# Performance work log

Hardware: AMD Instinct MI355X
Metric: run time of the kernel (lower is better)

The kernel has to match this reference:

```python
import jax, jax.numpy as jnp
import numpy as np
from jax.ops import segment_sum
import math

N = 100_000
E = 1_600_000
D = 128          # node_feature_dim
HID = 128        # hidden_dim
H = 4            # num_heads
HD = HID // H    # head_dim


def setup_inputs() -> dict:
    key = jax.random.key(0)
    ks = jax.random.split(key, 12)
    s = 0.02
    return {
        "node_features": jax.random.normal(ks[0], (N, D), dtype=jnp.float32),
        "edge_index": jax.random.randint(ks[1], (2, E), 0, N, dtype=jnp.int32),
        "edge_weights": jax.random.uniform(ks[2], (E,), dtype=jnp.float32),
        "Wq": jax.random.normal(ks[3], (D, HID), dtype=jnp.float32) * s,
        "bq": jnp.zeros((HID,), dtype=jnp.float32),
        "Wk": jax.random.normal(ks[4], (D, HID), dtype=jnp.float32) * s,
        "bk": jnp.zeros((HID,), dtype=jnp.float32),
        "Wv": jax.random.normal(ks[5], (D, HID), dtype=jnp.float32) * s,
        "bv": jnp.zeros((HID,), dtype=jnp.float32),
        "Wo": jax.random.normal(ks[6], (HID, HID), dtype=jnp.float32) * s,
        "bo": jnp.zeros((HID,), dtype=jnp.float32),
        "We": jax.random.normal(ks[7], (H,), dtype=jnp.float32) * s,  # edge_proj weight, Linear(1, H)
        "be": jnp.zeros((H,), dtype=jnp.float32),
    }


def reference(node_features, edge_index, edge_weights,
              Wq, bq, Wk, bk, Wv, bv, Wo, bo, We, be):
    scale = math.sqrt(HD)
    Q = (node_features @ Wq + bq).reshape(N, H, HD)
    K = (node_features @ Wk + bk).reshape(N, H, HD)
    V = (node_features @ Wv + bv).reshape(N, H, HD)

    src, tgt = edge_index[0], edge_index[1]

    # per-edge attention scores (E, H)
    scores = jnp.einsum("ehd,ehd->eh", Q[tgt], K[src]) / scale
    # edge_proj: Linear(1, H) applied to edge_weights[:, None]
    scores = scores + edge_weights[:, None] * We[None, :] + be[None, :]

    # scatter softmax over target nodes
    max_scores = jnp.full((N, H), -1e9, dtype=scores.dtype).at[tgt].max(scores)
    exp_scores = jnp.exp(scores - max_scores[tgt])
    sum_exp = segment_sum(exp_scores, tgt, num_segments=N)
    probs = exp_scores / (sum_exp[tgt] + 1e-8)

    # weighted scatter-sum aggregation
    out = jnp.zeros((N, H, HD), dtype=scores.dtype).at[tgt].add(probs[:, :, None] * V[src])
    return out.reshape(N, HID) @ Wo + bo
```

## Files before the change

kernel.cpp:

```cpp
#include <hip/hip_runtime.h>

#define N_NODES 100000
#define E_EDGES 1600000

typedef unsigned short u16;
typedef unsigned int   u32;
typedef unsigned char  u8;
typedef float f32x4  __attribute__((ext_vector_type(4)));
typedef short bf16x8 __attribute__((ext_vector_type(8)));

#define NBUK 98
#define BCAP 20480
#define MBLOCKS 1563
#define ECHUNKS 391

__device__ __forceinline__ u16 f2b(float f) {
  u32 b = __float_as_uint(f);
  return (u16)((b + 0x7FFFu + ((b >> 16) & 1u)) >> 16);
}
__device__ __forceinline__ float blo(u32 u) { return __uint_as_float(u << 16); }
__device__ __forceinline__ float bhi(u32 u) { return __uint_as_float(u & 0xFFFF0000u); }

__device__ __forceinline__ u8 f2e4m3(float f) {
  u32 b = __float_as_uint(f);
  u32 s = (b >> 24) & 0x80u;
  float y = __uint_as_float(b & 0x7fffffffu) * 0x1p-120f;
  u32 u = __float_as_uint(y);
  u += 0x7FFFFu + ((u >> 20) & 1u);
  return (u8)(s | ((u >> 20) & 0x7fu));
}

__device__ __forceinline__ float e4m3_1(u32 x) {
  u32 y = ((x & 0x80u) << 24) | ((x & 0x7fu) << 20);
  return __uint_as_float(y) * 0x1p120f;
}

__device__ __forceinline__ void dec4(u32 kq, float& k0, float& k1, float& k2, float& k3) {
#if __has_builtin(__builtin_amdgcn_cvt_pk_f32_fp8)
  auto lo = __builtin_amdgcn_cvt_pk_f32_fp8((int)kq, false);
  auto hi = __builtin_amdgcn_cvt_pk_f32_fp8((int)kq, true);
  k0 = lo[0]; k1 = lo[1]; k2 = hi[0]; k3 = hi[1];
#else
  k0 = e4m3_1(kq); k1 = e4m3_1(kq >> 8); k2 = e4m3_1(kq >> 16); k3 = e4m3_1(kq >> 24);
#endif
}

template<int CTRL>
__device__ __forceinline__ float dpp_add(float d) {
  int x = __builtin_amdgcn_update_dpp(0, __float_as_int(d), CTRL, 0xf, 0xf, true);
  return d + __int_as_float(x);
}
__device__ __forceinline__ float reduce8(float d) {
  d = dpp_add<0xB1>(d);
  d = dpp_add<0x4E>(d);
  d = dpp_add<0x141>(d);
  return d;
}

__global__ __launch_bounds__(256) void setup(
    const float* __restrict__ Wq, const float* __restrict__ Wk,
    const float* __restrict__ Wv, const float* __restrict__ Wo,
    u16* __restrict__ Wt, u32* __restrict__ bcur)
{
  int tid = blockIdx.x * 256 + threadIdx.x;
  if (tid < NBUK) bcur[tid] = (u32)tid * BCAP;
  int idx = tid - NBUK;
  if (idx >= 0 && idx < 65536) {
    int mat = idx >> 14;
    int rem = idx & 16383;
    int n = rem >> 7, k = rem & 127;
    const float* W = (mat == 0) ? Wq : (mat == 1) ? Wk : (mat == 2) ? Wv : Wo;
    Wt[idx] = f2b(W[k * 128 + n]);
  }
}

__global__ __launch_bounds__(256) void qkv_pass1(
    const float* __restrict__ A, const u16* __restrict__ Wt,
    const float* __restrict__ bq, const float* __restrict__ bk,
    const float* __restrict__ bv,
    u16* __restrict__ Qb, u8* __restrict__ Kf8, u16* __restrict__ Vb16, int M,
    const int* __restrict__ ei, const float* __restrict__ ew,
    u32* __restrict__ bcur, uint2* __restrict__ stag)
{
  __shared__ __align__(16) char smem[52224];
  const int t = threadIdx.x;

  if ((int)blockIdx.x < MBLOCKS) {
    typedef u16 row136[136];
    row136* Alds = (row136*)smem;
    row136* Blds = (row136*)(smem + 17408);
    const int row0 = blockIdx.x * 64;

#pragma unroll
    for (int i = 0; i < 8; ++i) {
      int f = t + i * 256;
      int r = f >> 5, c4 = f & 31;
      int gr = row0 + r; if (gr >= M) gr = M - 1;
      float4 v = ((const float4*)(A + (size_t)gr * 128))[c4];
      u32* dst = (u32*)&Alds[r][c4 * 4];
      dst[0] = (u32)f2b(v.x) | ((u32)f2b(v.y) << 16);
      dst[1] = (u32)f2b(v.z) | ((u32)f2b(v.w) << 16);
    }

    const int lane = t & 63;
    const int mrow = lane & 15;
    const int q    = lane >> 4;
    const int m0   = (t >> 6) * 16;

    for (int m = 0; m < 3; ++m) {
      __syncthreads();
#pragma unroll
      for (int i = 0; i < 8; ++i) {
        int f = t + i * 256;
        int r = f >> 4, c8 = f & 15;
        uint4 v = ((const uint4*)(Wt + (size_t)m * 16384 + (size_t)r * 128))[c8];
        *(uint4*)&Blds[r][c8 * 8] = v;
      }
      __syncthreads();

      f32x4 acc[8];
#pragma unroll
      for (int c = 0; c < 8; ++c) acc[c] = (f32x4){0.f, 0.f, 0.f, 0.f};
#pragma unroll
      for (int kk = 0; kk < 4; ++kk) {
        const int kb = kk * 32 + q * 8;
        bf16x8 a = *(const bf16x8*)&Alds[m0 + mrow][kb];
#pragma unroll
        for (int c = 0; c < 8; ++c) {
          bf16x8 b = *(const bf16x8*)&Blds[c * 16 + mrow][kb];
          acc[c] = __builtin_amdgcn_mfma_f32_16x16x32_bf16(a, b, acc[c], 0, 0, 0);
        }
      }

      const float* bias = (m == 0) ? bq : (m == 1) ? bk : bv;
      __syncthreads();
      if (m == 1) {
        u8* Kst = (u8*)Blds;
#pragma unroll
        for (int c = 0; c < 8; ++c) {
          int gcol = c * 16 + mrow;
          float bvv = bias[gcol];
#pragma unroll
          for (int r = 0; r < 4; ++r)
            Kst[(m0 + q * 4 + r) * 128 + gcol] = f2e4m3(acc[c][r] + bvv);
        }
        __syncthreads();
#pragma unroll
        for (int i = 0; i < 2; ++i) {
          int f = t + i * 256;
          int r = f >> 3, c16 = f & 7;
          int grow = row0 + r;
          if (grow < M)
            *(uint4*)(Kf8 + (size_t)grow * 128 + c16 * 16) =
                *(const uint4*)(Kst + r * 128 + c16 * 16);
        }
      } else {
        u16* St = (u16*)Blds;
#pragma unroll
        for (int c = 0; c < 8; ++c) {
          int gcol = c * 16 + mrow;
          float bvv = bias[gcol];
#pragma unroll
          for (int r = 0; r < 4; ++r)
            St[(m0 + q * 4 + r) * 128 + gcol] = f2b(acc[c][r] + bvv);
        }
        __syncthreads();
        u16* dstM = (m == 0) ? Qb : Vb16;
#pragma unroll
        for (int i = 0; i < 4; ++i) {
          int f = t + i * 256;
          int r = f >> 4, c8 = f & 15;
          int grow = row0 + r;
          if (grow < M)
            *(uint4*)(dstM + (size_t)grow * 128 + c8 * 8) =
                *(const uint4*)(St + r * 128 + c8 * 8);
        }
      }
    }
  } else {
    u32* s_px    = (u32*)smem;
    u32* s_py    = (u32*)(smem + 16384);
    u32* s_gp    = (u32*)(smem + 32768);
    u32* s_hist  = (u32*)(smem + 49152);
    u32* s_excl  = (u32*)(smem + 49544);
    u32* s_gbase = (u32*)(smem + 49936);
    u32* s_wsum  = (u32*)(smem + 50328);

    const int base = ((int)blockIdx.x - MBLOCKS) * 4096;
    const int nv = min(4096, E_EDGES - base);

    if (t < NBUK) s_hist[t] = 0;
    __syncthreads();

    u32 tg[16], py[16];
    const int4*   src4 = (const int4*)(ei + base);
    const int4*   tgt4 = (const int4*)(ei + E_EDGES + base);
    const float4* ewv4 = (const float4*)(ew + base);
#pragma unroll
    for (int j = 0; j < 4; ++j) {
      int q4 = t + j * 256;
      bool valid = (q4 * 4) < nv;
      int qq = valid ? q4 : 0;
      int4   sv = src4[qq];
      int4   tv = tgt4[qq];
      float4 wv = ewv4[qq];
      u32* TG = &tg[j * 4];
      u32* PY = &py[j * 4];
      TG[0] = (u32)tv.x; TG[1] = (u32)tv.y; TG[2] = (u32)tv.z; TG[3] = (u32)tv.w;
      PY[0] = ((u32)sv.x << 15) | (u32)(wv.x * 32768.0f);
      PY[1] = ((u32)sv.y << 15) | (u32)(wv.y * 32768.0f);
      PY[2] = ((u32)sv.z << 15) | (u32)(wv.z * 32768.0f);
      PY[3] = ((u32)sv.w << 15) | (u32)(wv.w * 32768.0f);
      if (valid) {
        atomicAdd(&s_hist[TG[0] >> 10], 1u);
        atomicAdd(&s_hist[TG[1] >> 10], 1u);
        atomicAdd(&s_hist[TG[2] >> 10], 1u);
        atomicAdd(&s_hist[TG[3] >> 10], 1u);
      } else {
        TG[0] = TG[1] = TG[2] = TG[3] = 0xFFFFFFFFu;
      }
    }
    __syncthreads();

    {
      int v = (t < NBUK) ? (int)s_hist[t] : 0;
      int x = v;
#pragma unroll
      for (int d = 1; d < 64; d <<= 1) {
        int y = __shfl_up(x, d, 64);
        if ((t & 63) >= d) x += y;
      }
      if ((t & 63) == 63 && t < 128) s_wsum[t >> 6] = (u32)x;
      __syncthreads();
      if (t < NBUK) {
        int incl = x + ((t >= 64) ? (int)s_wsum[0] : 0);
        s_excl[t] = (u32)(incl - v);
        s_gbase[t] = (v > 0) ? atomicAdd(&bcur[t], (u32)v) : 0u;
      }
    }
    __syncthreads();
    if (t < NBUK) s_hist[t] = s_excl[t];
    __syncthreads();

#pragma unroll
    for (int i = 0; i < 16; ++i) {
      if (tg[i] != 0xFFFFFFFFu) {
        u32 bk = tg[i] >> 10;
        u32 lp = atomicAdd(&s_hist[bk], 1u);
        s_px[lp] = tg[i];
        s_py[lp] = py[i];
        s_gp[lp] = s_gbase[bk] + (lp - s_excl[bk]);
      }
    }
    __syncthreads();
    for (int s = t; s < nv; s += 256)
      stag[s_gp[s]] = make_uint2(s_px[s], s_py[s]);
  }
}

__global__ __launch_bounds__(256) void gemm_out(
    const u16* __restrict__ A, const u16* __restrict__ Wt,
    const float* __restrict__ bias, float* __restrict__ Cout, int M)
{
  __shared__ __align__(16) u16 Alds[64][136];
  __shared__ __align__(16) u16 Blds[128][136];
  const int t = threadIdx.x;
  const int row0 = blockIdx.x * 64;

#pragma unroll
  for (int i = 0; i < 4; ++i) {
    int f = t + i * 256;
    int r = f >> 4, c8 = f & 15;
    int gr = row0 + r; if (gr >= M) gr = M - 1;
    uint4 v = ((const uint4*)(A + (size_t)gr * 128))[c8];
    *(uint4*)&Alds[r][c8 * 8] = v;
  }
#pragma unroll
  for (int i = 0; i < 8; ++i) {
    int f = t + i * 256;
    int r = f >> 4, c8 = f & 15;
    uint4 v = ((const uint4*)(Wt + (size_t)r * 128))[c8];
    *(uint4*)&Blds[r][c8 * 8] = v;
  }
  __syncthreads();

  const int lane = t & 63;
  const int mrow = lane & 15;
  const int q    = lane >> 4;
  const int m0   = (t >> 6) * 16;

  f32x4 acc[8];
#pragma unroll
  for (int c = 0; c < 8; ++c) acc[c] = (f32x4){0.f, 0.f, 0.f, 0.f};
#pragma unroll
  for (int kk = 0; kk < 4; ++kk) {
    const int kb = kk * 32 + q * 8;
    bf16x8 a = *(const bf16x8*)&Alds[m0 + mrow][kb];
#pragma unroll
    for (int c = 0; c < 8; ++c) {
      bf16x8 b = *(const bf16x8*)&Blds[c * 16 + mrow][kb];
      acc[c] = __builtin_amdgcn_mfma_f32_16x16x32_bf16(a, b, acc[c], 0, 0, 0);
    }
  }

  __syncthreads();
  float* Fst = (float*)&Blds[0][0];
#pragma unroll
  for (int c = 0; c < 8; ++c) {
    int gcol = c * 16 + mrow;
    float bv = bias[gcol];
#pragma unroll
    for (int r = 0; r < 4; ++r)
      Fst[(m0 + q * 4 + r) * 132 + gcol] = acc[c][r] + bv;
  }
  __syncthreads();
#pragma unroll
  for (int i = 0; i < 8; ++i) {
    int f = t + i * 256;
    int r = f >> 5, c4 = f & 31;
    int grow = row0 + r;
    if (grow < M)
      *(float4*)(Cout + (size_t)grow * 128 + c4 * 4) =
          *(const float4*)(Fst + r * 132 + c4 * 4);
  }
}

__global__ __launch_bounds__(1024) void pass2_scatter(
    const u32* __restrict__ bcur, const uint2* __restrict__ stag,
    int2* __restrict__ nodeinfo, u32* __restrict__ csr)
{
  __shared__ int s_hist[1024];
  __shared__ int s_wsum[16];
  const int t = threadIdx.x;
  const int b = blockIdx.x;
  const int sb = b * BCAP;
  const int cnt = (int)bcur[b] - sb;
  const int node_base = b << 10;

  s_hist[t] = 0;
  __syncthreads();

  u32 tgr[20], pyr[20];
#pragma unroll
  for (int k = 0; k < 20; ++k) {
    int i = t + k * 1024;
    if (i < cnt) {
      uint2 e = stag[sb + i];
      tgr[k] = e.x & 1023u;
      pyr[k] = e.y;
      atomicAdd(&s_hist[tgr[k]], 1);
    } else {
      tgr[k] = 0xFFFFFFFFu;
      pyr[k] = 0u;
    }
  }
  __syncthreads();

  int v = s_hist[t];
  int x = v;
#pragma unroll
  for (int d = 1; d < 64; d <<= 1) {
    int y = __shfl_up(x, d, 64);
    if ((t & 63) >= d) x += y;
  }
  if ((t & 63) == 63) s_wsum[t >> 6] = x;
  __syncthreads();
  if (t < 64) {
    int w = (t < 16) ? s_wsum[t] : 0;
#pragma unroll
    for (int d = 1; d < 16; d <<= 1) {
      int y = __shfl_up(w, d, 64);
      if (t >= d) w += y;
    }
    if (t < 16) s_wsum[t] = w;
  }
  __syncthreads();
  int wbase = (t >= 64) ? s_wsum[(t >> 6) - 1] : 0;
  int excl = x + wbase - v;
  int node = node_base + t;
  if (node < N_NODES) nodeinfo[node] = make_int2(sb + excl, v);
  __syncthreads();
  s_hist[t] = sb + excl;
  __syncthreads();

#pragma unroll
  for (int k = 0; k < 20; ++k) {
    if (tgr[k] != 0xFFFFFFFFu) {
      int pos = atomicAdd(&s_hist[tgr[k]], 1);
      csr[pos] = pyr[k];
    }
  }
}

__global__ __launch_bounds__(256) void gather_fused(
    const int2* __restrict__ nodeinfo, const u32* __restrict__ csr,
    u32* __restrict__ Qb32, const u8* __restrict__ Kf8,
    const u32* __restrict__ Vb,
    const float* __restrict__ We, const float* __restrict__ be)
{
  int node = blockIdx.x * 4 + (threadIdx.x >> 6);
  int l    = threadIdx.x & 63;
  int half = l >> 5;
  int hl   = l & 31;
  int h    = hl >> 3;

  const float scale = 0.17677669529663687f;
  const float eiq   = 1.0f / 32768.0f;
  uint2 qp = *(const uint2*)(Qb32 + (size_t)node * 64 + hl * 2);
  float qa = blo(qp.x) * scale, qb = bhi(qp.x) * scale;
  float qc = blo(qp.y) * scale, qd = bhi(qp.y) * scale;
  float weq = We[h] * eiq, bE = be[h];
  const u32 laneK = (u32)hl * 4;
  const u32 laneV = (u32)hl * 8;

  int2 ni = nodeinfo[node];
  int s0 = ni.x, L = ni.y;
  int npair = L >> 1;
  const u32* cp = csr + s0 + half;
  const char* Kc = (const char*)Kf8;
  const char* Vc = (const char*)Vb;

  float a0 = 0.f, a1 = 0.f, a2 = 0.f, a3 = 0.f, sum = 0.f;

  auto LDK = [&](u32 c) -> u32 {
    return *(const u32*)(Kc + (((c >> 15) << 7) + laneK));
  };
  auto LDV = [&](u32 c) -> uint2 {
    return *(const uint2*)(Vc + (((c >> 15) << 8) + laneV));
  };
  auto COMP = [&](u32 c, u32 kq, uint2 vv) {
    float k0, k1, k2, k3;
    dec4(kq, k0, k1, k2, k3);
    float d = qa * k0 + qb * k1 + qc * k2 + qd * k3;
    d = reduce8(d);
    float p = __expf(d + (float)(c & 32767u) * weq + bE);
    sum += p;
    a0 += p * blo(vv.x);
    a1 += p * bhi(vv.x);
    a2 += p * blo(vv.y);
    a3 += p * bhi(vv.y);
  };

  int i = 0;
  for (; i + 4 <= npair; i += 4) {
    u32 c0 = cp[2 * i];
    u32 c1 = cp[2 * i + 2];
    u32 c2 = cp[2 * i + 4];
    u32 c3 = cp[2 * i + 6];
    u32 k0 = LDK(c0), k1 = LDK(c1), k2 = LDK(c2), k3 = LDK(c3);
    uint2 v0 = LDV(c0), v1 = LDV(c1), v2 = LDV(c2), v3 = LDV(c3);
    COMP(c0, k0, v0);
    COMP(c1, k1, v1);
    COMP(c2, k2, v2);
    COMP(c3, k3, v3);
  }
  for (; i < npair; ++i) {
    u32 c = cp[2 * i];
    u32 kq = LDK(c);
    uint2 vv = LDV(c);
    COMP(c, kq, vv);
  }
  if (L & 1) {
    u32 c = csr[s0 + L - 1];
    u32 kq = LDK(c);
    uint2 vv = LDV(c);
    float k0, k1, k2, k3;
    dec4(kq, k0, k1, k2, k3);
    float d = qa * k0 + qb * k1 + qc * k2 + qd * k3;
    d = reduce8(d);
    float p = __expf(d + (float)(c & 32767u) * weq + bE);
    p = half ? 0.f : p;
    sum += p;
    a0 += p * blo(vv.x);
    a1 += p * bhi(vv.x);
    a2 += p * blo(vv.y);
    a3 += p * bhi(vv.y);
  }

  sum += __shfl_xor(sum, 32, 64);
  a0  += __shfl_xor(a0, 32, 64);
  a1  += __shfl_xor(a1, 32, 64);
  a2  += __shfl_xor(a2, 32, 64);
  a3  += __shfl_xor(a3, 32, 64);

  float inv = 1.f / (sum + 1e-8f);
  if (half == 0) {
    uint2 w;
    w.x = (u32)f2b(a0 * inv) | ((u32)f2b(a1 * inv) << 16);
    w.y = (u32)f2b(a2 * inv) | ((u32)f2b(a3 * inv) << 16);
    *(uint2*)(Qb32 + (size_t)node * 64 + hl * 2) = w;
  }
}

extern "C" void kernel_launch(void* const* d_in, const int* in_sizes, int n_in,
                              void* d_out, int out_size, void* d_ws, size_t ws_size,
                              hipStream_t stream) {
  const float* nf = (const float*)d_in[0];
  const int*   ei = (const int*)  d_in[1];
  const float* ew = (const float*)d_in[2];
  const float* Wq = (const float*)d_in[3];
  const float* bq = (const float*)d_in[4];
  const float* Wk = (const float*)d_in[5];
  const float* bk = (const float*)d_in[6];
  const float* Wv = (const float*)d_in[7];
  const float* bv = (const float*)d_in[8];
  const float* Wo = (const float*)d_in[9];
  const float* bo = (const float*)d_in[10];
  const float* We = (const float*)d_in[11];
  const float* be = (const float*)d_in[12];
  float* out = (float*)d_out;

  char* ws = (char*)d_ws;
  u16*  Wt  = (u16*)ws;
  u16*  Qb  = (u16*)(ws + 131072);
  u8*   Kf8 = (u8*)(Qb + (size_t)N_NODES * 128);
  u16*  Vb16 = (u16*)(Kf8 + (size_t)N_NODES * 128);
  char* p   = (char*)(Vb16 + (size_t)N_NODES * 128);
  uint2* stag = (uint2*)p;              p += (size_t)NBUK * BCAP * 8;
  u32*  csr = (u32*)p;                  p += (size_t)NBUK * BCAP * 4;
  int2* nodeinfo = (int2*)p;            p += (size_t)N_NODES * 8;
  u32*  bcur = (u32*)p;                 p += 512;

  setup<<<(NBUK + 65536 + 255) / 256, 256, 0, stream>>>(Wq, Wk, Wv, Wo, Wt, bcur);

  qkv_pass1<<<MBLOCKS + ECHUNKS, 256, 0, stream>>>(
      nf, Wt, bq, bk, bv, Qb, Kf8, Vb16, N_NODES, ei, ew, bcur, stag);

  pass2_scatter<<<NBUK, 1024, 0, stream>>>(bcur, stag, nodeinfo, csr);

  gather_fused<<<N_NODES / 4, 256, 0, stream>>>(nodeinfo, csr,
      (u32*)Qb, Kf8, (const u32*)Vb16, We, be);

  gemm_out<<<MBLOCKS, 256, 0, stream>>>(Qb, Wt + 49152, bo, out, N_NODES);
}
```

Baseline: 275.3 us.

## Compute per-node degrees in pass1 and stream staging in pass2 scatter

```diff
diff --git a/kernel.cpp b/kernel.cpp
--- a/kernel.cpp
+++ b/kernel.cpp
@@ -13,6 +13,7 @@
 #define BCAP 20480
 #define MBLOCKS 1563
 #define ECHUNKS 391
+#define NDPAD 100352
 
 __device__ __forceinline__ u16 f2b(float f) {
   u32 b = __float_as_uint(f);
@@ -80,7 +81,8 @@
     const float* __restrict__ bv,
     u16* __restrict__ Qb, u8* __restrict__ Kf8, u16* __restrict__ Vb16, int M,
     const int* __restrict__ ei, const float* __restrict__ ew,
-    u32* __restrict__ bcur, uint2* __restrict__ stag)
+    u32* __restrict__ bcur, uint2* __restrict__ stag,
+    u32* __restrict__ nodedeg)
 {
   __shared__ __align__(16) char smem[52224];
   const int t = threadIdx.x;
@@ -107,14 +109,29 @@
     const int q    = lane >> 4;
     const int m0   = (t >> 6) * 16;
 
+    uint4 wreg[8], wnxt[8];
+#pragma unroll
+    for (int i = 0; i < 8; ++i) {
+      int f = t + i * 256;
+      int r = f >> 4, c8 = f & 15;
+      wreg[i] = ((const uint4*)(Wt + (size_t)r * 128))[c8];
+    }
+
     for (int m = 0; m < 3; ++m) {
       __syncthreads();
 #pragma unroll
       for (int i = 0; i < 8; ++i) {
         int f = t + i * 256;
         int r = f >> 4, c8 = f & 15;
-        uint4 v = ((const uint4*)(Wt + (size_t)m * 16384 + (size_t)r * 128))[c8];
-        *(uint4*)&Blds[r][c8 * 8] = v;
+        *(uint4*)&Blds[r][c8 * 8] = wreg[i];
+      }
+      if (m < 2) {
+#pragma unroll
+        for (int i = 0; i < 8; ++i) {
+          int f = t + i * 256;
+          int r = f >> 4, c8 = f & 15;
+          wnxt[i] = ((const uint4*)(Wt + (size_t)(m + 1) * 16384 + (size_t)r * 128))[c8];
+        }
       }
       __syncthreads();
 
@@ -176,6 +193,8 @@
                 *(const uint4*)(St + r * 128 + c8 * 8);
         }
       }
+#pragma unroll
+      for (int i = 0; i < 8; ++i) wreg[i] = wnxt[i];
     }
   } else {
     u32* s_px    = (u32*)smem;
@@ -216,6 +235,10 @@
         atomicAdd(&s_hist[TG[1] >> 10], 1u);
         atomicAdd(&s_hist[TG[2] >> 10], 1u);
         atomicAdd(&s_hist[TG[3] >> 10], 1u);
+        atomicAdd(&nodedeg[TG[0]], 1u);
+        atomicAdd(&nodedeg[TG[1]], 1u);
+        atomicAdd(&nodedeg[TG[2]], 1u);
+        atomicAdd(&nodedeg[TG[3]], 1u);
       } else {
         TG[0] = TG[1] = TG[2] = TG[3] = 0xFFFFFFFFu;
       }
@@ -319,44 +342,29 @@
     int f = t + i * 256;
     int r = f >> 5, c4 = f & 31;
     int grow = row0 + r;
-    if (grow < M)
-      *(float4*)(Cout + (size_t)grow * 128 + c4 * 4) =
-          *(const float4*)(Fst + r * 132 + c4 * 4);
+    if (grow < M) {
+      f32x4 vv = *(const f32x4*)(Fst + r * 132 + c4 * 4);
+      __builtin_nontemporal_store(vv, (f32x4*)(Cout + (size_t)grow * 128 + c4 * 4));
+    }
   }
 }
 
 __global__ __launch_bounds__(1024) void pass2_scatter(
-    const u32* __restrict__ bcur, const uint2* __restrict__ stag,
+    const u32* __restrict__ bcur, const u32* __restrict__ nodedeg,
+    const uint2* __restrict__ stag,
     int2* __restrict__ nodeinfo, u32* __restrict__ csr)
 {
-  __shared__ int s_hist[1024];
+  __shared__ int s_cur[1024];
   __shared__ int s_wsum[16];
   const int t = threadIdx.x;
   const int b = blockIdx.x;
   const int sb = b * BCAP;
   const int cnt = (int)bcur[b] - sb;
   const int node_base = b << 10;
-
-  s_hist[t] = 0;
-  __syncthreads();
-
-  u32 tgr[20], pyr[20];
-#pragma unroll
-  for (int k = 0; k < 20; ++k) {
-    int i = t + k * 1024;
-    if (i < cnt) {
-      uint2 e = stag[sb + i];
-      tgr[k] = e.x & 1023u;
-      pyr[k] = e.y;
-      atomicAdd(&s_hist[tgr[k]], 1);
-    } else {
-      tgr[k] = 0xFFFFFFFFu;
-      pyr[k] = 0u;
-    }
-  }
-  __syncthreads();
-
-  int v = s_hist[t];
+  const int node = node_base + t;
+
+  int v = (int)nodedeg[node];
+
   int x = v;
 #pragma unroll
   for (int d = 1; d < 64; d <<= 1) {
@@ -377,18 +385,31 @@
   __syncthreads();
   int wbase = (t >= 64) ? s_wsum[(t >> 6) - 1] : 0;
   int excl = x + wbase - v;
-  int node = node_base + t;
   if (node < N_NODES) nodeinfo[node] = make_int2(sb + excl, v);
+  s_cur[t] = sb + excl;
   __syncthreads();
-  s_hist[t] = sb + excl;
-  __syncthreads();
-
-#pragma unroll
-  for (int k = 0; k < 20; ++k) {
-    if (tgr[k] != 0xFFFFFFFFu) {
-      int pos = atomicAdd(&s_hist[tgr[k]], 1);
-      csr[pos] = pyr[k];
-    }
+
+  typedef unsigned long long u64;
+  const u64* sg = (const u64*)stag;
+  int i = t;
+  for (; i + 3072 < cnt; i += 4096) {
+    u64 e0 = __builtin_nontemporal_load(sg + sb + i);
+    u64 e1 = __builtin_nontemporal_load(sg + sb + i + 1024);
+    u64 e2 = __builtin_nontemporal_load(sg + sb + i + 2048);
+    u64 e3 = __builtin_nontemporal_load(sg + sb + i + 3072);
+    int p0 = atomicAdd(&s_cur[(u32)e0 & 1023u], 1);
+    int p1 = atomicAdd(&s_cur[(u32)e1 & 1023u], 1);
+    int p2 = atomicAdd(&s_cur[(u32)e2 & 1023u], 1);
+    int p3 = atomicAdd(&s_cur[(u32)e3 & 1023u], 1);
+    csr[p0] = (u32)(e0 >> 32);
+    csr[p1] = (u32)(e1 >> 32);
+    csr[p2] = (u32)(e2 >> 32);
+    csr[p3] = (u32)(e3 >> 32);
+  }
+  for (; i < cnt; i += 1024) {
+    u64 e = __builtin_nontemporal_load(sg + sb + i);
+    int pos = atomicAdd(&s_cur[(u32)e & 1023u], 1);
+    csr[pos] = (u32)(e >> 32);
   }
 }
 
@@ -520,13 +541,16 @@
   u32*  csr = (u32*)p;                  p += (size_t)NBUK * BCAP * 4;
   int2* nodeinfo = (int2*)p;            p += (size_t)N_NODES * 8;
   u32*  bcur = (u32*)p;                 p += 512;
+  u32*  nodedeg = (u32*)p;              p += (size_t)NDPAD * 4;
+
+  hipMemsetAsync(nodedeg, 0, (size_t)NDPAD * 4, stream);
 
   setup<<<(NBUK + 65536 + 255) / 256, 256, 0, stream>>>(Wq, Wk, Wv, Wo, Wt, bcur);
 
   qkv_pass1<<<MBLOCKS + ECHUNKS, 256, 0, stream>>>(
-      nf, Wt, bq, bk, bv, Qb, Kf8, Vb16, N_NODES, ei, ew, bcur, stag);
-
-  pass2_scatter<<<NBUK, 1024, 0, stream>>>(bcur, stag, nodeinfo, csr);
+      nf, Wt, bq, bk, bv, Qb, Kf8, Vb16, N_NODES, ei, ew, bcur, stag, nodedeg);
+
+  pass2_scatter<<<NBUK, 1024, 0, stream>>>(bcur, nodedeg, stag, nodeinfo, csr);
 
   gather_fused<<<N_NODES / 4, 256, 0, stream>>>(nodeinfo, csr,
       (u32*)Qb, Kf8, (const u32*)Vb16, We, be);
```

Measured after the change: 408.2 us. 1.48x slower.
